# Kernel optimization log

Measured on AMD Instinct MI355X. Metric: run time of the kernel, lower is better.

The kernel has to match this reference:

```python
import jax, jax.numpy as jnp
import numpy as np

EPS = 1e-6
CHUNK = 256
N_HEADS = 16
GATE_NORM = 16.0


def rmsnorm(x, eps=EPS):
    # RMSNorm without affine; normalizes over the last axis (matches custom
    # RMSNorm applied pre-view over full dim for q/k/v and over head_dim for subln)
    return x * jax.lax.rsqrt(jnp.mean(x * x, axis=-1, keepdims=True) + eps)


def chunk_gate_retention(q, k, v, gt, chunk_size):
    """Chunked gated linear attention (RetNet/GLA-style).
    Recurrence: S_t = exp(g_t) * S_{t-1} + k_t^T v_t;  o_t = q_t @ S_t.
    q,k,v: (b,h,t,d); gt: (b,h,t) log-decay. Returns (o, last_state)."""
    b, h, t, d = q.shape
    c = chunk_size
    n = t // c
    scale = d ** -0.5
    q = q.reshape(b, h, n, c, d) * scale
    k = k.reshape(b, h, n, c, d)
    v = v.reshape(b, h, n, c, d)
    g = gt.reshape(b, h, n, c)
    bc = jnp.cumsum(g, axis=-1)            # cumulative log-decay within chunk (incl. own gate)
    B = bc[..., -1:]                        # total chunk log-decay (b,h,n,1)
    # ---- intra-chunk (causal, decayed) ----
    decay = jnp.exp(bc[..., :, None] - bc[..., None, :])  # (b,h,n,c,c), <=1 on/below diag
    mask = jnp.tril(jnp.ones((c, c), dtype=bool))
    A = jnp.einsum('bhnid,bhnjd->bhnij', q, k) * jnp.where(mask, decay, 0.0)
    o_intra = jnp.einsum('bhnij,bhnjd->bhnid', A, v)
    # ---- per-chunk kv summaries (decay from position j to chunk end) ----
    kd = k * jnp.exp(B - bc)[..., None]
    kv = jnp.einsum('bhncd,bhnce->bhnde', kd, v)          # (b,h,n,d,d)
    qd = q * jnp.exp(bc)[..., None]                        # state decay into position i
    # ---- inter-chunk recurrence over chunk index ----
    def step(S, inp):
        qd_n, kv_n, B_n = inp
        o_cross = jnp.einsum('bhcd,bhde->bhce', qd_n, S)
        S_new = jnp.exp(B_n)[..., None] * S + kv_n
        return S_new, o_cross
    S0 = jnp.zeros((b, h, d, d), dtype=q.dtype)
    inps = (jnp.moveaxis(qd, 2, 0), jnp.moveaxis(kv, 2, 0), jnp.moveaxis(B, 2, 0))
    S_last, o_cross = jax.lax.scan(step, S0, inps)
    o_cross = jnp.moveaxis(o_cross, 0, 2)                  # (b,h,n,c,d)
    o = (o_intra + o_cross).reshape(b, h, t, d)
    return o, S_last


def setup_inputs() -> dict:
    key = jax.random.key(0)
    ks = jax.random.split(key, 7)
    dim, nh = 1024, N_HEADS
    s = 0.03  # keep activations sane
    return {
        'x':   jax.random.normal(ks[0], (2, 8192, dim), dtype=jnp.float32),
        'Wq':  jax.random.normal(ks[1], (dim, dim), dtype=jnp.float32) * s,
        'Wk':  jax.random.normal(ks[2], (dim, dim), dtype=jnp.float32) * s,
        'Wv':  jax.random.normal(ks[3], (dim, dim), dtype=jnp.float32) * s,
        'Wg':  jax.random.normal(ks[4], (dim, dim), dtype=jnp.float32) * s,
        'Wgt': jax.random.normal(ks[5], (dim, nh), dtype=jnp.float32) * s,
        'Wo':  jax.random.normal(ks[6], (dim, dim), dtype=jnp.float32) * s,
    }


def reference(x, Wq, Wk, Wv, Wg, Wgt, Wo):
    b, t, dim = x.shape
    h = N_HEADS
    d = dim // h
    q = rmsnorm(x @ Wq)
    k = rmsnorm(x @ Wk)
    v = rmsnorm(x @ Wv)
    g = x @ Wg
    gt = jax.nn.log_sigmoid(x @ Wgt) / GATE_NORM   # (b,t,h)
    qr = q.reshape(b, t, h, d).transpose(0, 2, 1, 3)
    kr = k.reshape(b, t, h, d).transpose(0, 2, 1, 3)
    vr = v.reshape(b, t, h, d).transpose(0, 2, 1, 3)
    gtr = gt.transpose(0, 2, 1)                    # (b,h,t)
    o, _ = chunk_gate_retention(qr, kr, vr, gtr, CHUNK)
    o = rmsnorm(o)                                 # subln over head_dim
    o = o.transpose(0, 2, 1, 3).reshape(b, t, dim)
    o = jax.nn.silu(g) * o                         # swiglu(g, o)
    return o @ Wo
```

## Files before the change

kernel.cpp:

```cpp
#include <hip/hip_runtime.h>

#define T_SEQ 8192
#define NH 16
#define HD 64
#define DIM 1024
#define ROWS 16384
#define CHK 256
#define NCHK 32

typedef float f32x4 __attribute__((ext_vector_type(4)));
typedef __bf16 bf16x8 __attribute__((ext_vector_type(8)));
typedef short short8 __attribute__((ext_vector_type(8)));
typedef short short4v __attribute__((ext_vector_type(4)));
typedef unsigned short ushort_t;

__device__ __forceinline__ float bf2f(ushort_t u){ return __uint_as_float(((unsigned)u)<<16); }
__device__ __forceinline__ ushort_t f2bf(float f){
  unsigned u = __float_as_uint(f);
  u += 0x7FFFu + ((u>>16)&1u);
  return (ushort_t)(u>>16);
}
#define BFLO(u) __uint_as_float((u)<<16)
#define BFHI(u) __uint_as_float((u)&0xFFFF0000u)
#define MFMA16(a,b,c) __builtin_amdgcn_mfma_f32_16x16x32_bf16((a),(b),(c),0,0,0)

__global__ __launch_bounds__(256) void transpose_all(const float* __restrict__ Wq,
    const float* __restrict__ Wk, const float* __restrict__ Wv,
    const float* __restrict__ Wg, const float* __restrict__ Wo,
    ushort_t* __restrict__ wcat, ushort_t* __restrict__ wot){
  int z = blockIdx.z;
  const float* W = (z==0)?Wq:(z==1)?Wk:(z==2)?Wv:(z==3)?Wg:Wo;
  ushort_t* D = (z<4)? (wcat + (size_t)z*DIM*DIM) : wot;
  __shared__ float tile[64][65];
  int k0 = blockIdx.x*64, n0 = blockIdx.y*64;
  int tid = threadIdx.x;
  #pragma unroll
  for (int it=0; it<16; ++it){
    int idx = tid + it*256;
    int r = idx>>6, c = idx&63;
    tile[r][c] = W[(size_t)(k0+r)*DIM + n0+c];
  }
  __syncthreads();
  #pragma unroll
  for (int it=0; it<16; ++it){
    int idx = tid + it*256;
    int r = idx>>6, c = idx&63;
    D[(size_t)(n0+r)*DIM + k0+c] = f2bf(tile[c][r]);
  }
}

template<int OUT_BF16>
__global__ __launch_bounds__(256,2) void gemm_bt(const ushort_t* __restrict__ A,
    const ushort_t* __restrict__ Bt, void* __restrict__ Cv, int M, int N, int K,
    float* __restrict__ ssqp, int yoff){
  __shared__ __align__(16) ushort_t As[128*64];
  __shared__ __align__(16) ushort_t Bs[128*64];
  int tid = threadIdx.x;
  int lane = tid & 63, wid = tid >> 6;
  int wr = wid >> 1, wc = wid & 1;
  int m0 = blockIdx.x * 128, n0 = blockIdx.y * 128;
  f32x4 acc[4][4] = {};
  int srow = tid >> 3;
  int sg = tid & 7;
  const int nkt = K >> 6;
  for (int kt = 0; kt < nkt; ++kt){
    short8 ra[4], rb[4];
    #pragma unroll
    for (int s = 0; s < 4; ++s){
      int row = s*32 + srow;
      int gl = sg ^ (row & 7);
      ra[s] = *(const short8*)&A[(size_t)(m0 + row)*K + kt*64 + gl*8];
      rb[s] = *(const short8*)&Bt[(size_t)(n0 + row)*K + kt*64 + gl*8];
    }
    __syncthreads();
    #pragma unroll
    for (int s = 0; s < 4; ++s){
      int row = s*32 + srow;
      *(short8*)&As[row*64 + sg*8] = ra[s];
      *(short8*)&Bs[row*64 + sg*8] = rb[s];
    }
    __syncthreads();
    #pragma unroll
    for (int kk = 0; kk < 2; ++kk){
      bf16x8 af[4], bfv[4];
      #pragma unroll
      for (int m = 0; m < 4; ++m){
        int row = wr*64 + m*16 + (lane & 15);
        int g = kk*4 + (lane >> 4);
        af[m] = *(const bf16x8*)&As[row*64 + ((g ^ (row & 7))<<3)];
      }
      #pragma unroll
      for (int n = 0; n < 4; ++n){
        int row = wc*64 + n*16 + (lane & 15);
        int g = kk*4 + (lane >> 4);
        bfv[n] = *(const bf16x8*)&Bs[row*64 + ((g ^ (row & 7))<<3)];
      }
      #pragma unroll
      for (int m = 0; m < 4; ++m)
        #pragma unroll
        for (int n = 0; n < 4; ++n)
          acc[m][n] = MFMA16(af[m], bfv[n], acc[m][n]);
    }
  }
  #pragma unroll
  for (int m = 0; m < 4; ++m){
    int row = m0 + wr*64 + m*16 + (lane>>4)*4;
    #pragma unroll
    for (int n = 0; n < 4; ++n){
      int col = n0 + wc*64 + n*16 + (lane & 15);
      #pragma unroll
      for (int r = 0; r < 4; ++r){
        float v = acc[m][n][r];
        if (OUT_BF16) ((ushort_t*)Cv)[(size_t)(row+r)*N + col] = f2bf(v);
        else          ((float*)Cv)[(size_t)(row+r)*N + col] = v;
      }
    }
  }
  if (OUT_BF16 && (yoff + (int)blockIdx.y) < 24){
    int slot = (yoff + blockIdx.y)*2 + wc;
    #pragma unroll
    for (int m = 0; m < 4; ++m){
      #pragma unroll
      for (int r = 0; r < 4; ++r){
        float s = 0.f;
        #pragma unroll
        for (int n = 0; n < 4; ++n){ float xx = acc[m][n][r]; s += xx*xx; }
        s += __shfl_xor(s,1); s += __shfl_xor(s,2);
        s += __shfl_xor(s,4); s += __shfl_xor(s,8);
        if ((lane & 15) == 0){
          int row = m0 + wr*64 + m*16 + (lane>>4)*4 + r;
          ssqp[(size_t)slot*ROWS + row] = s;
        }
      }
    }
  }
}

__global__ __launch_bounds__(256) void rms_combine(const float* __restrict__ ssqp,
                                                   float* __restrict__ rmsb){
  int idx = blockIdx.x*256 + threadIdx.x;
  int mat = idx >> 14, row = idx & (ROWS-1);
  float s = 0.f;
  #pragma unroll
  for (int k=0;k<16;++k) s += ssqp[(size_t)(mat*16+k)*ROWS + row];
  rmsb[idx] = rsqrtf(s*(1.f/1024.f)+1e-6f);
}

__global__ __launch_bounds__(256) void gt_ker(const float* __restrict__ x,
    const float* __restrict__ Wgt, float* __restrict__ gtb, ushort_t* __restrict__ xbf){
  int row = blockIdx.x; int b = row>>13; int t = row & (T_SEQ-1);
  int tid = threadIdx.x; int lane = tid&63; int w = tid>>6;
  __shared__ float xs[1024];
  #pragma unroll
  for (int i=0;i<4;++i) xs[tid+256*i] = x[(size_t)row*DIM + tid+256*i];
  __syncthreads();
  short4v xb4;
  #pragma unroll
  for (int k2=0;k2<4;++k2) xb4[k2] = (short)f2bf(xs[tid*4+k2]);
  *(short4v*)&xbf[(size_t)row*DIM + tid*4] = xb4;
  float a0=0,a1=0,a2=0,a3=0;
  #pragma unroll
  for (int jj=0;jj<16;++jj){
    int j = lane + 64*jj;
    float xv = xs[j];
    const float* wp = &Wgt[(size_t)j*NH + w*4];
    a0 += xv*wp[0]; a1 += xv*wp[1]; a2 += xv*wp[2]; a3 += xv*wp[3];
  }
  #pragma unroll
  for (int off=32; off>=1; off>>=1){
    a0 += __shfl_xor(a0, off); a1 += __shfl_xor(a1, off);
    a2 += __shfl_xor(a2, off); a3 += __shfl_xor(a3, off);
  }
  if (lane==0){
    float za[4] = {a0,a1,a2,a3};
    #pragma unroll
    for (int i=0;i<4;++i){
      float z = za[i];
      float ls = fminf(z,0.f) - log1pf(__expf(-fabsf(z)));
      gtb[((size_t)(b*NH + w*4 + i))*T_SEQ + t] = ls * (1.f/16.f);
    }
  }
}

__global__ __launch_bounds__(512,2) void attn_p1(const ushort_t* __restrict__ qkvg,
    const float* __restrict__ gtb, const float* __restrict__ rmsb,
    float* __restrict__ Bb, ushort_t* __restrict__ kvb){
  __shared__ __align__(16) ushort_t sh2[32768];
  __shared__ float bcf[256];
  __shared__ float tmp4[4];
  ushort_t* kdt = sh2;
  ushort_t* vt  = sh2 + 16384;
  int bid = blockIdx.x; int n = bid&31; int bh = bid>>5; int b = bh>>4; int h = bh&15;
  int t0 = n*CHK; int tid = threadIdx.x; int lane = tid&63; int w = tid>>6;
  float vscan = 0.f;
  if (tid < 256){
    vscan = gtb[(size_t)bh*T_SEQ + t0 + tid];
    #pragma unroll
    for (int off=1; off<64; off<<=1){ float u = __shfl_up(vscan, off); if (lane>=off) vscan += u; }
    if (lane==63) tmp4[w] = vscan;
  }
  __syncthreads();
  float Bn = tmp4[0]+tmp4[1]+tmp4[2]+tmp4[3];
  if (tid < 256){
    float pre=0;
    #pragma unroll
    for (int i=0;i<4;++i) if (i<w) pre += tmp4[i];
    bcf[tid] = vscan + pre;
  }
  if (tid==0) Bb[bid] = Bn;
  __syncthreads();
  {
    int j = tid>>1, dh = tid&1;
    int grow = b*T_SEQ + t0 + j;
    size_t rowb = (size_t)grow*4096;
    float fk = rmsb[ROWS + grow] * __expf(Bn - bcf[j]);
    float fv = rmsb[2*ROWS + grow];
    #pragma unroll
    for (int q8=0; q8<4; ++q8){
      short8 k8 = *(const short8*)&qkvg[rowb + 1024 + h*HD + dh*32 + q8*8];
      short8 v8 = *(const short8*)&qkvg[rowb + 2048 + h*HD + dh*32 + q8*8];
      #pragma unroll
      for (int kk=0; kk<8; ++kk){
        int d = dh*32 + q8*8 + kk;
        kdt[(d<<8) + (((j>>3)^(d&7))<<3) + (j&7)] = f2bf(bf2f((ushort_t)k8[kk])*fk);
        vt [(d<<8) + (((j>>3)^(d&7))<<3) + (j&7)] = f2bf(bf2f((ushort_t)v8[kk])*fv);
      }
    }
  }
  __syncthreads();
  if (w < 4){
    f32x4 acc[4] = {};
    #pragma unroll
    for (int s=0; s<8; ++s){
      int d = w*16 + (lane&15);
      int jj = s*32 + (lane>>4)*8;
      bf16x8 ka = *(const bf16x8*)&kdt[(d<<8) + (((jj>>3)^(d&7))<<3)];
      #pragma unroll
      for (int et=0; et<4; ++et){
        int e = et*16 + (lane&15);
        bf16x8 vf = *(const bf16x8*)&vt[(e<<8) + (((jj>>3)^(e&7))<<3)];
        acc[et] = MFMA16(ka, vf, acc[et]);
      }
    }
    ushort_t* kvp = &kvb[(size_t)bid*4096];
    #pragma unroll
    for (int et=0; et<4; ++et)
      #pragma unroll
      for (int r=0; r<4; ++r)
        kvp[(et*16 + (lane&15))*64 + w*16 + (lane>>4)*4 + r] = f2bf(acc[et][r]);
  }
}

__global__ __launch_bounds__(256) void scan_ker(const ushort_t* __restrict__ kvb,
    const float* __restrict__ Bb, ushort_t* __restrict__ Sb){
  int gidx = blockIdx.x*256 + threadIdx.x;
  int bh = gidx >> 12; int f = gidx & 4095;
  float S = 0.f;
  const ushort_t* kp = &kvb[(size_t)bh*NCHK*4096 + f];
  ushort_t* sp = &Sb[(size_t)bh*NCHK*4096 + f];
  for (int n=0;n<NCHK;++n){
    sp[(size_t)n*4096] = f2bf(S);
    S = __expf(Bb[bh*NCHK+n])*S + bf2f(kp[(size_t)n*4096]);
  }
}

__global__ __launch_bounds__(512,2) void attn_p3(const ushort_t* __restrict__ qkvg,
    const float* __restrict__ gtb, const float* __restrict__ rmsb,
    const ushort_t* __restrict__ Sb, ushort_t* __restrict__ oact){
  __shared__ __align__(16) ushort_t sh[(32768+16384+1024+32+2048)/2];
  ushort_t* vt = sh;
  ushort_t* ps = sh + 16384;
  float* bcs = (float*)(sh + 24576);
  float* tmp = (float*)(sh + 25088);
  float* rqs = (float*)(sh + 25104);
  float* rks = (float*)(sh + 25616);
  int bid = blockIdx.x; int n = bid&31; int bh = bid>>5; int b = bh>>4; int h = bh&15;
  int t0 = n*CHK; int tid = threadIdx.x; int lane = tid&63; int w = tid>>6;
  int wrow = w*32;
  size_t chunkbase = (size_t)b*T_SEQ + t0;
  int qcol = lane & 15, hi = lane >> 4;
  bf16x8 qf[2][2];
  #pragma unroll
  for (int rt=0; rt<2; ++rt)
    #pragma unroll
    for (int s=0; s<2; ++s)
      qf[rt][s] = *(const bf16x8*)&qkvg[(chunkbase + wrow + rt*16 + qcol)*4096
                                        + h*HD + s*32 + hi*8];
  float vscan = 0.f;
  if (tid < 256){
    vscan = gtb[(size_t)bh*T_SEQ + t0 + tid];
    #pragma unroll
    for (int off=1; off<64; off<<=1){ float u = __shfl_up(vscan, off); if (lane>=off) vscan += u; }
    if (lane==63) tmp[w] = vscan;
  }
  __syncthreads();
  if (tid < 256){
    float pre=0;
    #pragma unroll
    for (int i=0;i<4;++i) if (i<w) pre += tmp[i];
    bcs[tid] = vscan + pre;
    int grow = b*T_SEQ + t0 + tid;
    rqs[tid] = rmsb[grow];
    rks[tid] = rmsb[ROWS + grow];
  }
  {
    int j = tid>>1, ehalf = tid&1;
    int grow = b*T_SEQ + t0 + j;
    size_t rowb = (size_t)grow*4096;
    float fv = rmsb[2*ROWS + grow];
    #pragma unroll
    for (int q8=0; q8<4; ++q8){
      short8 v8 = *(const short8*)&qkvg[rowb + 2048 + h*HD + ehalf*32 + q8*8];
      #pragma unroll
      for (int kk=0; kk<8; ++kk){
        int e = ehalf*32 + q8*8 + kk;
        vt[(e<<8) + (((j>>3)^(e&7))<<3) + (j&7)] = f2bf(bf2f((ushort_t)v8[kk])*fv);
      }
    }
  }
  __syncthreads();
  f32x4 o_[2][4] = {};
  #pragma unroll
  for (int s=0; s<2; ++s)
    #pragma unroll
    for (int et=0; et<4; ++et){
      bf16x8 stf = *(const bf16x8*)&Sb[(size_t)bid*4096 + (et*16 + qcol)*64 + s*32 + hi*8];
      #pragma unroll
      for (int rt=0; rt<2; ++rt)
        o_[rt][et] = MFMA16(qf[rt][s], stf, o_[rt][et]);
    }
  #pragma unroll
  for (int rt=0; rt<2; ++rt)
    #pragma unroll
    for (int rr=0; rr<4; ++rr){
      int ri = wrow + rt*16 + hi*4 + rr;
      float fs = 0.125f*__expf(bcs[ri])*rqs[ri];
      #pragma unroll
      for (int et=0; et<4; ++et) o_[rt][et][rr] *= fs;
    }
  float rqv[2], bqv[2];
  #pragma unroll
  for (int rt=0; rt<2; ++rt){
    int qr = wrow + rt*16 + qcol;
    rqv[rt] = rqs[qr]; bqv[rt] = bcs[qr];
  }
  int s0 = qcol + 32*(hi&1), s1 = s0 + 16;
  bool ctp = (hi >> 1) != 0;
  for (int hb=0; hb<=w; ++hb){
    int jbase = hb*32;
    bool dia = (hb == w);
    bf16x8 kf[2][2];
    #pragma unroll
    for (int s=0; s<2; ++s)
      #pragma unroll
      for (int ct=0; ct<2; ++ct)
        kf[s][ct] = *(const bf16x8*)&qkvg[(chunkbase + jbase + ct*16 + qcol)*4096
                                          + 1024 + h*HD + s*32 + hi*8];
    f32x4 s2[2][2] = {};
    #pragma unroll
    for (int s=0; s<2; ++s)
      #pragma unroll
      for (int ct=0; ct<2; ++ct)
        #pragma unroll
        for (int rt=0; rt<2; ++rt)
          s2[rt][ct] = MFMA16(kf[s][ct], qf[rt][s], s2[rt][ct]);
    bf16x8 vf[4];
    #pragma unroll
    for (int et=0; et<4; ++et){
      int e = et*16 + qcol;
      int jj = jbase + hi*8;
      vf[et] = *(const bf16x8*)&vt[(e<<8) + (((jj>>3) ^ (e&7))<<3)];
    }
    #pragma unroll
    for (int rt=0; rt<2; ++rt){
      int qr = wrow + rt*16 + qcol;
      unsigned wd[2][2];
      #pragma unroll
      for (int ct=0; ct<2; ++ct){
        float pv[4];
        #pragma unroll
        for (int rr=0; rr<4; ++rr){
          int kr = jbase + ct*16 + hi*4 + rr;
          float val = s2[rt][ct][rr] * 0.125f * rqv[rt] * rks[kr] * __expf(bqv[rt] - bcs[kr]);
          if (dia && kr > qr) val = 0.f;
          pv[rr] = val;
        }
        wd[ct][0] = ((unsigned)f2bf(pv[1])<<16) | f2bf(pv[0]);
        wd[ct][1] = ((unsigned)f2bf(pv[3])<<16) | f2bf(pv[2]);
      }
      unsigned a00 = (unsigned)__shfl((int)wd[0][0], s0);
      unsigned a10 = (unsigned)__shfl((int)wd[1][0], s0);
      unsigned a01 = (unsigned)__shfl((int)wd[0][1], s0);
      unsigned a11 = (unsigned)__shfl((int)wd[1][1], s0);
      unsigned b00 = (unsigned)__shfl((int)wd[0][0], s1);
      unsigned b10 = (unsigned)__shfl((int)wd[1][0], s1);
      unsigned b01 = (unsigned)__shfl((int)wd[0][1], s1);
      unsigned b11 = (unsigned)__shfl((int)wd[1][1], s1);
      union { unsigned u[4]; bf16x8 v; } pa;
      pa.u[0] = ctp ? a10 : a00;
      pa.u[1] = ctp ? a11 : a01;
      pa.u[2] = ctp ? b10 : b00;
      pa.u[3] = ctp ? b11 : b01;
      #pragma unroll
      for (int et=0; et<4; ++et)
        o_[rt][et] = MFMA16(pa.v, vf[et], o_[rt][et]);
    }
  }
  float rms8[2][4];
  #pragma unroll
  for (int rt=0; rt<2; ++rt)
    #pragma unroll
    for (int rr=0; rr<4; ++rr){
      float ssq = 0.f;
      #pragma unroll
      for (int et=0; et<4; ++et){ float xx = o_[rt][et][rr]; ssq += xx*xx; }
      ssq += __shfl_xor(ssq,1); ssq += __shfl_xor(ssq,2);
      ssq += __shfl_xor(ssq,4); ssq += __shfl_xor(ssq,8);
      rms8[rt][rr] = rsqrtf(ssq*(1.f/64.f)+1e-6f);
    }
  #pragma unroll
  for (int eh=0; eh<2; ++eh){
    #pragma unroll
    for (int rt=0; rt<2; ++rt)
      #pragma unroll
      for (int e2=0; e2<2; ++e2){
        int et = eh*2 + e2;
        #pragma unroll
        for (int rr=0; rr<4; ++rr){
          int pi = rt*16 + hi*4 + rr;
          int pj = e2*16 + qcol;
          ps[w*1024 + pi*32 + (((pj>>3) ^ ((pi>>2)&3))<<3) + (pj&7)] =
            f2bf(o_[rt][et][rr]*rms8[rt][rr]);
        }
      }
    int i2 = lane&31, e16 = (lane>>5)*16;
    int gr0 = e16>>3;
    int f = (i2>>2)&3;
    short8 ov0 = *(const short8*)&ps[w*1024 + i2*32 + ((gr0^f)<<3)];
    short8 ov1 = *(const short8*)&ps[w*1024 + i2*32 + (((gr0+1)^f)<<3)];
    size_t rowg = chunkbase + wrow + i2;
    short8 gv0 = *(const short8*)&qkvg[rowg*4096 + 3072 + h*HD + eh*32 + e16];
    short8 gv1 = *(const short8*)&qkvg[rowg*4096 + 3072 + h*HD + eh*32 + e16 + 8];
    ushort_t outv[16];
    #pragma unroll
    for (int k=0;k<8;++k){
      float gf = bf2f((ushort_t)gv0[k]);
      float sg = gf/(1.f+__expf(-gf));
      outv[k] = f2bf(bf2f((ushort_t)ov0[k])*sg);
    }
    #pragma unroll
    for (int k=0;k<8;++k){
      float gf = bf2f((ushort_t)gv1[k]);
      float sg = gf/(1.f+__expf(-gf));
      outv[8+k] = f2bf(bf2f((ushort_t)ov1[k])*sg);
    }
    ushort_t* op = &oact[rowg*DIM + h*HD + eh*32 + e16];
    *(short8*)&op[0] = *(short8*)&outv[0];
    *(short8*)&op[8] = *(short8*)&outv[8];
  }
}

extern "C" void kernel_launch(void* const* d_in, const int* in_sizes, int n_in,
                              void* d_out, int out_size, void* d_ws, size_t ws_size,
                              hipStream_t stream){
  const float* x  = (const float*)d_in[0];
  const float* Wq = (const float*)d_in[1];
  const float* Wk = (const float*)d_in[2];
  const float* Wv = (const float*)d_in[3];
  const float* Wg = (const float*)d_in[4];
  const float* Wgt= (const float*)d_in[5];
  const float* Wo = (const float*)d_in[6];
  float* out = (float*)d_out;

  char* p = (char*)d_ws;
  ushort_t* xbf  = (ushort_t*)p; p += (size_t)ROWS*DIM*2;
  ushort_t* wcat = (ushort_t*)p; p += (size_t)4*DIM*DIM*2;
  ushort_t* wot  = (ushort_t*)p; p += (size_t)DIM*DIM*2;
  ushort_t* qkvg = (ushort_t*)p; p += (size_t)ROWS*4096*2;
  float* gtb = (float*)p; p += (size_t)32*T_SEQ*4;
  float* Bb  = (float*)p; p += 1024*4;
  ushort_t* kvb = (ushort_t*)p; p += (size_t)1024*4096*2;
  ushort_t* Sb = (ushort_t*)p; p += (size_t)1024*4096*2;
  ushort_t* oact = (ushort_t*)p; p += (size_t)ROWS*DIM*2;
  float* ssqp = (float*)p; p += (size_t)48*ROWS*4;
  float* rmsb = (float*)p; p += (size_t)3*ROWS*4;
  if ((size_t)(p - (char*)d_ws) > ws_size) return;

  gt_ker<<<ROWS,256,0,stream>>>(x, Wgt, gtb, xbf);
  transpose_all<<<dim3(16,16,5),256,0,stream>>>(Wq, Wk, Wv, Wg, Wo, wcat, wot);
  gemm_bt<1><<<dim3(ROWS/128, 16), 256, 0, stream>>>(xbf, wcat, qkvg, ROWS, 4096, DIM, ssqp, 0);
  gemm_bt<1><<<dim3(ROWS/128, 16), 256, 0, stream>>>(xbf, wcat + (size_t)2048*DIM,
                                                     qkvg + 2048, ROWS, 4096, DIM, ssqp, 16);
  rms_combine<<<(3*ROWS)/256,256,0,stream>>>(ssqp, rmsb);
  attn_p1<<<1024,512,0,stream>>>(qkvg, gtb, rmsb, Bb, kvb);
  scan_ker<<<512,256,0,stream>>>(kvb, Bb, Sb);
  attn_p3<<<1024,512,0,stream>>>(qkvg, gtb, rmsb, Sb, oact);
  gemm_bt<0><<<dim3(ROWS/128, 1024/128), 256, 0, stream>>>(oact, wot, out, ROWS, 1024, DIM, nullptr, 0);
}
```

Baseline: 384.1 us.

## Compute gate logits with MFMA in a tiled cast kernel and merge QKVG GEMM launches

Replaces the per-row scalar gate kernel with a 64-row tiled kernel that casts x to bf16 and computes x@Wgt with bf16 MFMA from LDS, using a transposed bf16 copy of Wgt. This cuts the launch count and the strided scalar Wgt reads. It also folds the two half-width projection GEMM launches into one full-width launch. The gate logits now use bf16 inputs instead of fp32, which slightly changes their precision, and each block re-converts the whole Wgt matrix.

```diff
diff --git a/kernel.cpp b/kernel.cpp
--- a/kernel.cpp
+++ b/kernel.cpp
@@ -46,6 +46,65 @@
     int idx = tid + it*256;
     int r = idx>>6, c = idx&63;
     D[(size_t)(n0+r)*DIM + k0+c] = f2bf(tile[c][r]);
+  }
+}
+
+__global__ __launch_bounds__(256,2) void cast_gt_ker(const float* __restrict__ x,
+    const float* __restrict__ Wgt, ushort_t* __restrict__ xbf, float* __restrict__ gtb){
+  __shared__ __align__(16) ushort_t As[64*64];
+  __shared__ __align__(16) ushort_t wgt_t[16*1040];
+  int tid = threadIdx.x, lane = tid&63, w = tid>>6;
+  int r0 = blockIdx.x*64;
+  #pragma unroll 4
+  for (int i=0;i<64;++i){
+    int idx = tid + i*256;
+    wgt_t[(idx&15)*1040 + (idx>>4)] = f2bf(Wgt[idx]);
+  }
+  int arow = tid>>2;
+  int acg = (tid&3)*2;
+  const float* xrow = &x[(size_t)(r0+arow)*1024 + (tid&3)*16];
+  ushort_t* xbrow = &xbf[(size_t)(r0+arow)*1024 + (tid&3)*16];
+  int aslot0 = ((acg   ^ (arow&7))<<3);
+  int aslot1 = (((acg+1) ^ (arow&7))<<3);
+  f32x4 acc = {0.f,0.f,0.f,0.f};
+  float4 f0 = *(const float4*)&xrow[0];
+  float4 f1 = *(const float4*)&xrow[4];
+  float4 f2 = *(const float4*)&xrow[8];
+  float4 f3 = *(const float4*)&xrow[12];
+  __syncthreads();
+  for (int kt=0; kt<16; ++kt){
+    ushort_t c[16] = { f2bf(f0.x),f2bf(f0.y),f2bf(f0.z),f2bf(f0.w),
+                       f2bf(f1.x),f2bf(f1.y),f2bf(f1.z),f2bf(f1.w),
+                       f2bf(f2.x),f2bf(f2.y),f2bf(f2.z),f2bf(f2.w),
+                       f2bf(f3.x),f2bf(f3.y),f2bf(f3.z),f2bf(f3.w) };
+    *(short8*)&xbrow[kt*64]   = *(short8*)&c[0];
+    *(short8*)&xbrow[kt*64+8] = *(short8*)&c[8];
+    *(short8*)&As[arow*64 + aslot0] = *(short8*)&c[0];
+    *(short8*)&As[arow*64 + aslot1] = *(short8*)&c[8];
+    if (kt < 15){
+      f0 = *(const float4*)&xrow[(kt+1)*64 + 0];
+      f1 = *(const float4*)&xrow[(kt+1)*64 + 4];
+      f2 = *(const float4*)&xrow[(kt+1)*64 + 8];
+      f3 = *(const float4*)&xrow[(kt+1)*64 +12];
+    }
+    __syncthreads();
+    #pragma unroll
+    for (int kk=0;kk<2;++kk){
+      int row = w*16 + (lane&15);
+      int g = kk*4 + (lane>>4);
+      bf16x8 af = *(const bf16x8*)&As[row*64 + ((g^(row&7))<<3)];
+      bf16x8 bfr = *(const bf16x8*)&wgt_t[(lane&15)*1040 + kt*64 + kk*32 + (lane>>4)*8];
+      acc = MFMA16(af, bfr, acc);
+    }
+    __syncthreads();
+  }
+  #pragma unroll
+  for (int r=0;r<4;++r){
+    int grow = r0 + w*16 + (lane>>4)*4 + r;
+    int bb = grow>>13, t = grow&(T_SEQ-1);
+    float z = acc[r];
+    float ls = fminf(z,0.f) - log1pf(__expf(-fabsf(z)));
+    gtb[((size_t)(bb*NH + (lane&15)))*T_SEQ + t] = ls*(1.f/16.f);
   }
 }
 
@@ -146,42 +205,6 @@
   rmsb[idx] = rsqrtf(s*(1.f/1024.f)+1e-6f);
 }
 
-__global__ __launch_bounds__(256) void gt_ker(const float* __restrict__ x,
-    const float* __restrict__ Wgt, float* __restrict__ gtb, ushort_t* __restrict__ xbf){
-  int row = blockIdx.x; int b = row>>13; int t = row & (T_SEQ-1);
-  int tid = threadIdx.x; int lane = tid&63; int w = tid>>6;
-  __shared__ float xs[1024];
-  #pragma unroll
-  for (int i=0;i<4;++i) xs[tid+256*i] = x[(size_t)row*DIM + tid+256*i];
-  __syncthreads();
-  short4v xb4;
-  #pragma unroll
-  for (int k2=0;k2<4;++k2) xb4[k2] = (short)f2bf(xs[tid*4+k2]);
-  *(short4v*)&xbf[(size_t)row*DIM + tid*4] = xb4;
-  float a0=0,a1=0,a2=0,a3=0;
-  #pragma unroll
-  for (int jj=0;jj<16;++jj){
-    int j = lane + 64*jj;
-    float xv = xs[j];
-    const float* wp = &Wgt[(size_t)j*NH + w*4];
-    a0 += xv*wp[0]; a1 += xv*wp[1]; a2 += xv*wp[2]; a3 += xv*wp[3];
-  }
-  #pragma unroll
-  for (int off=32; off>=1; off>>=1){
-    a0 += __shfl_xor(a0, off); a1 += __shfl_xor(a1, off);
-    a2 += __shfl_xor(a2, off); a3 += __shfl_xor(a3, off);
-  }
-  if (lane==0){
-    float za[4] = {a0,a1,a2,a3};
-    #pragma unroll
-    for (int i=0;i<4;++i){
-      float z = za[i];
-      float ls = fminf(z,0.f) - log1pf(__expf(-fabsf(z)));
-      gtb[((size_t)(b*NH + w*4 + i))*T_SEQ + t] = ls * (1.f/16.f);
-    }
-  }
-}
-
 __global__ __launch_bounds__(512,2) void attn_p1(const ushort_t* __restrict__ qkvg,
     const float* __restrict__ gtb, const float* __restrict__ rmsb,
     float* __restrict__ Bb, ushort_t* __restrict__ kvb){
@@ -486,11 +509,9 @@
   float* rmsb = (float*)p; p += (size_t)3*ROWS*4;
   if ((size_t)(p - (char*)d_ws) > ws_size) return;
 
-  gt_ker<<<ROWS,256,0,stream>>>(x, Wgt, gtb, xbf);
+  cast_gt_ker<<<ROWS/64,256,0,stream>>>(x, Wgt, xbf, gtb);
   transpose_all<<<dim3(16,16,5),256,0,stream>>>(Wq, Wk, Wv, Wg, Wo, wcat, wot);
-  gemm_bt<1><<<dim3(ROWS/128, 16), 256, 0, stream>>>(xbf, wcat, qkvg, ROWS, 4096, DIM, ssqp, 0);
-  gemm_bt<1><<<dim3(ROWS/128, 16), 256, 0, stream>>>(xbf, wcat + (size_t)2048*DIM,
-                                                     qkvg + 2048, ROWS, 4096, DIM, ssqp, 16);
+  gemm_bt<1><<<dim3(ROWS/128, 4096/128), 256, 0, stream>>>(xbf, wcat, qkvg, ROWS, 4096, DIM, ssqp, 0);
   rms_combine<<<(3*ROWS)/256,256,0,stream>>>(ssqp, rmsb);
   attn_p1<<<1024,512,0,stream>>>(qkvg, gtb, rmsb, Bb, kvb);
   scan_ker<<<512,256,0,stream>>>(kvb, Bb, Sb);
```

Measured after the change: 320.7 us (median of 2 runs). -16.5%, faster.
